# Performance work log

Hardware: AMD Instinct MI355X
Metric: run time of the kernel (lower is better)

Reference implementation:

```python
import jax, jax.numpy as jnp
import numpy as np

HEAD_SIZE = 64


def setup_inputs() -> dict:
    key = jax.random.key(0)
    k1, k2, k3, k4 = jax.random.split(key, 4)
    B, T, C = 4, 4096, 1024
    x = jax.random.normal(k1, (B, T, C), dtype=jnp.float32)
    s = 1.0 / np.sqrt(C)  # ~kaiming-uniform scale for Linear weights
    Wk = jax.random.normal(k2, (C, HEAD_SIZE), dtype=jnp.float32) * s
    Wq = jax.random.normal(k3, (C, HEAD_SIZE), dtype=jnp.float32) * s
    Wv = jax.random.normal(k4, (C, HEAD_SIZE), dtype=jnp.float32) * s
    return {"x": x, "Wk": Wk, "Wq": Wq, "Wv": Wv}


def reference(x, Wk, Wq, Wv):
    # x: [B,T,C]; Wk/Wq/Wv: [C,H]
    B, T, C = x.shape
    H = Wk.shape[1]
    k = jnp.einsum('btc,ch->bth', x, Wk)
    q = jnp.einsum('btc,ch->bth', x, Wq)
    v = jnp.einsum('btc,ch->bth', x, Wv)
    scale = 1.0 / jnp.sqrt(jnp.asarray(H, dtype=x.dtype))
    scores = jnp.einsum('bqh,bkh->bqk', q, k) * scale  # [B,T,T]
    causal = jnp.tril(jnp.ones((T, T), dtype=bool))
    scores = jnp.where(causal, scores, jnp.asarray(-jnp.inf, dtype=scores.dtype))
    attn = jax.nn.softmax(scores, axis=-1)
    out = jnp.einsum('bqk,bkh->bqh', attn, v)  # [B,T,H]
    return out
```

## Files before the change

kernel.cpp:

```cpp
#include <hip/hip_runtime.h>
#include <hip/hip_bf16.h>

#define T_ 4096
#define C_ 1024
#define H_ 64
#define LSTR 72
#define XBS 1032

typedef short bf16x8 __attribute__((ext_vector_type(8)));
typedef float f32x4 __attribute__((ext_vector_type(4)));

__device__ __forceinline__ short f2bf(float f) {
  union { __hip_bfloat16 h; short s; } u;
  u.h = __float2bfloat16(f);
  return u.s;
}
__device__ __forceinline__ unsigned pack2(float a, float b) {
  return ((unsigned)(unsigned short)f2bf(b) << 16) | (unsigned short)f2bf(a);
}

__global__ void wtrans_kernel(const float* __restrict__ Wk,
                              const float* __restrict__ Wq,
                              const float* __restrict__ Wv,
                              __hip_bfloat16* __restrict__ Wtf) {
  int tid = blockIdx.x * 256 + threadIdx.x;
  const int j = tid & 7;
  const int lane = (tid >> 3) & 63;
  const int m = lane & 15;
  const int quad = lane >> 4;
  const int f = (tid >> 9) & 15;
  const int nt = f & 3;
  const int ks = f >> 2;
  const int c = (tid >> 13) & 7;
  const int which = tid >> 16;
  const float* W = (which == 0) ? Wk : ((which == 1) ? Wq : Wv);
  const int cc = c * 128 + ks * 32 + quad * 8 + j;
  const int h = nt * 16 + m;
  Wtf[tid] = __float2bfloat16(W[cc * 64 + h]);
}

__global__ __launch_bounds__(256) void proj_kernel(
    const float* __restrict__ x, const __hip_bfloat16* __restrict__ Wtf,
    __hip_bfloat16* __restrict__ qb, __hip_bfloat16* __restrict__ Kf,
    __hip_bfloat16* __restrict__ Vf) {
  __shared__ __hip_bfloat16 Xb[16 * XBS];
  const int tid = threadIdx.x;
  const int lane = tid & 63;
  const int wave = tid >> 6;
  const int m = lane & 15;
  const int quad = lane >> 4;
  const int t0 = blockIdx.x * 16;

  const float4* xtile = (const float4*)(x + (size_t)t0 * C_);
  float4 xv[16];
#pragma unroll
  for (int k = 0; k < 16; ++k) xv[k] = xtile[tid + k * 256];
#pragma unroll
  for (int k = 0; k < 16; ++k) {
    const int idx = tid + k * 256;
    const int row = idx >> 8;
    const int c4 = idx & 255;
    uint2 u = {pack2(xv[k].x, xv[k].y), pack2(xv[k].z, xv[k].w)};
    *(uint2*)(&Xb[row * XBS + c4 * 4]) = u;
  }
  __syncthreads();

  int whichs[3], ntls[3];
  const __hip_bfloat16* wb[3];
#pragma unroll
  for (int i = 0; i < 3; ++i) {
    const int g = wave * 3 + i;
    whichs[i] = g >> 2;
    ntls[i] = g & 3;
    wb[i] = Wtf + (size_t)whichs[i] * 65536 + ntls[i] * 512 + lane * 8;
  }
  f32x4 acc[3];
#pragma unroll
  for (int i = 0; i < 3; ++i) acc[i] = (f32x4){0.f, 0.f, 0.f, 0.f};

#pragma unroll
  for (int c = 0; c < 8; ++c) {
    bf16x8 bq[12];
#pragma unroll
    for (int i = 0; i < 3; ++i)
#pragma unroll
      for (int ks = 0; ks < 4; ++ks)
        bq[i * 4 + ks] = *(const bf16x8*)(wb[i] + (c * 16 + ks * 4) * 512);
#pragma unroll
    for (int ks = 0; ks < 4; ++ks) {
      bf16x8 a = *(const bf16x8*)(&Xb[m * XBS + c * 128 + ks * 32 + quad * 8]);
#pragma unroll
      for (int i = 0; i < 3; ++i)
        acc[i] = __builtin_amdgcn_mfma_f32_16x16x32_bf16(a, bq[i * 4 + ks],
                                                         acc[i], 0, 0, 0);
    }
  }

  const int bb = t0 >> 12;
  const int tloc = t0 & (T_ - 1);
  const int ktile = tloc >> 6;
  const float cscale = 0.18033688011112042f;

#pragma unroll
  for (int i = 0; i < 3; ++i) {
    const int which = whichs[i];
    const int ntl = ntls[i];
    if (which == 1) {
#pragma unroll
      for (int r = 0; r < 4; ++r)
        qb[(size_t)(t0 + quad * 4 + r) * H_ + ntl * 16 + m] =
            __float2bfloat16(acc[i][r] * cscale);
    } else if (which == 0) {
      __hip_bfloat16* dst = Kf + ((size_t)bb * 64 + ktile) * 4096;
      const int ntK = (tloc >> 4) & 3;
      const int wh = ntl >> 1;
      const int quadK = (ntl * 2 + (m >> 3)) & 3;
      const int j = m & 7;
#pragma unroll
      for (int r = 0; r < 4; ++r) {
        const int mK = quad * 4 + r;
        dst[(ntK * 2 + wh) * 512 + (quadK * 16 + mK) * 8 + j] =
            __float2bfloat16(acc[i][r]);
      }
    } else {
      __hip_bfloat16* dst = Vf + ((size_t)bb * 64 + ktile) * 4096;
#pragma unroll
      for (int r = 0; r < 4; ++r) {
        const int kvo = (tloc & 63) + quad * 4 + r;
        const int half = (kvo >> 5) & 1;
        const int quadV = (kvo >> 3) & 3;
        const int j = kvo & 7;
        dst[(ntl * 2 + half) * 512 + (quadV * 16 + m) * 8 + j] =
            __float2bfloat16(acc[i][r]);
      }
    }
  }
}

__global__ __launch_bounds__(256, 4) void fa_pass1(
    const __hip_bfloat16* __restrict__ qg, const __hip_bfloat16* __restrict__ Kf,
    const __hip_bfloat16* __restrict__ Vf, float* __restrict__ Opart,
    float* __restrict__ Ml) {
  __shared__ __hip_bfloat16 Pl[4][16 * LSTR];
  const int lane = threadIdx.x & 63;
  const int wave = threadIdx.x >> 6;
  const int m = lane & 15;
  const int quad = lane >> 4;

  const int jid = blockIdx.x * 4 + wave;
  const int b = jid / 1152;
  const int j2 = jid - b * 1152;
  int g = 7;
  while (16 * g * (g + 1) > j2) --g;
  const int r2 = j2 - 16 * g * (g + 1);
  const int qt = 32 * g + r2 / (g + 1);
  const int c = r2 - (r2 / (g + 1)) * (g + 1);
  const int q0 = qt * 16;
  const int k0s = c * 512;
  const int kend0 = k0s + 512;
  const int kend = (kend0 < q0 + 16) ? kend0 : (q0 + 16);
  const int ntile = (kend - k0s + 63) >> 6;

  const __hip_bfloat16* qbase = qg + ((size_t)b * T_ + q0 + m) * H_;
  bf16x8 qf0 = *(const bf16x8*)(qbase + quad * 8);
  bf16x8 qf1 = *(const bf16x8*)(qbase + 32 + quad * 8);

  f32x4 Oacc[4];
#pragma unroll
  for (int i = 0; i < 4; ++i) Oacc[i] = (f32x4){0.f, 0.f, 0.f, 0.f};
  float psum = 0.f;

  const __hip_bfloat16* kgf = Kf + (size_t)b * 262144 + lane * 8;
  const __hip_bfloat16* vgf = Vf + (size_t)b * 262144 + lane * 8;
  __hip_bfloat16* Plw = &Pl[wave][0];

  for (int it = 0; it < ntile; ++it) {
    const int ktile = (k0s >> 6) + it;
    const int k0 = ktile * 64;
    const __hip_bfloat16* kp = kgf + (size_t)ktile * 4096;
    const __hip_bfloat16* vp = vgf + (size_t)ktile * 4096;

    f32x4 s[4];
#pragma unroll
    for (int nt = 0; nt < 4; ++nt) {
      bf16x8 kf0 = *(const bf16x8*)(kp + nt * 1024);
      bf16x8 kf1 = *(const bf16x8*)(kp + nt * 1024 + 512);
      f32x4 t = (f32x4){0.f, 0.f, 0.f, 0.f};
      t = __builtin_amdgcn_mfma_f32_16x16x32_bf16(kf0, qf0, t, 0, 0, 0);
      t = __builtin_amdgcn_mfma_f32_16x16x32_bf16(kf1, qf1, t, 0, 0, 0);
      s[nt] = t;
    }
    bf16x8 vf[8];
#pragma unroll
    for (int nt = 0; nt < 4; ++nt) {
      vf[2 * nt] = *(const bf16x8*)(vp + nt * 1024);
      vf[2 * nt + 1] = *(const bf16x8*)(vp + nt * 1024 + 512);
    }

    const bool needmask = (k0 + 63 > q0);
#pragma unroll
    for (int nt = 0; nt < 4; ++nt) {
      float p[4];
#pragma unroll
      for (int r = 0; r < 4; ++r) {
        float sv = s[nt][r];
        if (needmask && (k0 + nt * 16 + quad * 4 + r) > (q0 + m))
          sv = -__builtin_inff();
        p[r] = exp2f(sv);
        psum += p[r];
      }
      uint2 u = {pack2(p[0], p[1]), pack2(p[2], p[3])};
      *(uint2*)(&Plw[m * LSTR + nt * 16 + quad * 4]) = u;
    }

    bf16x8 pf0 = *(const bf16x8*)(&Plw[m * LSTR + quad * 8]);
    bf16x8 pf1 = *(const bf16x8*)(&Plw[m * LSTR + 32 + quad * 8]);
#pragma unroll
    for (int nt = 0; nt < 4; ++nt) {
      Oacc[nt] = __builtin_amdgcn_mfma_f32_16x16x32_bf16(pf0, vf[2 * nt], Oacc[nt], 0, 0, 0);
      Oacc[nt] = __builtin_amdgcn_mfma_f32_16x16x32_bf16(pf1, vf[2 * nt + 1], Oacc[nt], 0, 0, 0);
    }
  }

  psum += __shfl_xor(psum, 16);
  psum += __shfl_xor(psum, 32);

  float* Op = Opart + (size_t)jid * 1024;
#pragma unroll
  for (int nt = 0; nt < 4; ++nt)
#pragma unroll
    for (int r = 0; r < 4; ++r)
      Op[(quad * 4 + r) * 64 + nt * 16 + m] = Oacc[nt][r];
  if (lane < 16) Ml[(size_t)jid * 16 + lane] = psum;
}

__global__ __launch_bounds__(256) void fa_combine(
    const float* __restrict__ Opart, const float* __restrict__ Ml,
    float* __restrict__ out) {
  const int bq = blockIdx.x;
  const int b = bq >> 8;
  const int qt = bq & 255;
  const int g = qt >> 5;
  const int nc = g + 1;
  const int jbase = b * 1152 + 16 * g * (g + 1) + (qt & 31) * nc;
  const int r = threadIdx.x >> 4;
  const int h0 = (threadIdx.x & 15) * 4;

  float4 O = {0.f, 0.f, 0.f, 0.f};
  float L = 0.f;
  for (int c = 0; c < nc; ++c) {
    L += Ml[(size_t)(jbase + c) * 16 + r];
    float4 o = *(const float4*)(Opart + (size_t)(jbase + c) * 1024 + r * 64 + h0);
    O.x += o.x; O.y += o.y; O.z += o.z; O.w += o.w;
  }
  float inv = 1.f / L;
  float4 res = {O.x * inv, O.y * inv, O.z * inv, O.w * inv};
  *(float4*)(out + ((size_t)b * T_ + qt * 16 + r) * H_ + h0) = res;
}

extern "C" void kernel_launch(void* const* d_in, const int* in_sizes, int n_in,
                              void* d_out, int out_size, void* d_ws, size_t ws_size,
                              hipStream_t stream) {
  const float* x = (const float*)d_in[0];
  const float* Wk = (const float*)d_in[1];
  const float* Wq = (const float*)d_in[2];
  const float* Wv = (const float*)d_in[3];
  float* out = (float*)d_out;
  char* ws = (char*)d_ws;
  __hip_bfloat16* Wtf = (__hip_bfloat16*)ws;
  __hip_bfloat16* qb = (__hip_bfloat16*)(ws + 393216);
  __hip_bfloat16* Kf = (__hip_bfloat16*)(ws + 2490368);
  __hip_bfloat16* Vf = (__hip_bfloat16*)(ws + 4587520);
  float* Opart = (float*)(ws + 6684672);
  float* Ml = (float*)(ws + 25559040);

  hipLaunchKernelGGL(wtrans_kernel, dim3(768), dim3(256), 0, stream, Wk, Wq, Wv, Wtf);
  hipLaunchKernelGGL(proj_kernel, dim3(1024), dim3(256), 0, stream, x, Wtf, qb, Kf, Vf);
  hipLaunchKernelGGL(fa_pass1, dim3(1152), dim3(256), 0, stream, qb, Kf, Vf, Opart, Ml);
  hipLaunchKernelGGL(fa_combine, dim3(1024), dim3(256), 0, stream, Opart, Ml, out);
}
```

Measured before the change: 144.9 us.

## Prefetch next K tile, double-buffer P, and combine partials with atomics

The attention pass now loads the next K tile into registers while computing the current one, and ping-pongs the per-wave P staging buffer in LDS. Split-K partial outputs and row sums are no longer written to a partials buffer and reduced by a combine kernel. They are atomically accumulated into a zeroed final buffer, and a simple normalize kernel divides by the sum. This adds a memset, lowers the occupancy hint from 4 to 3, and relies on float atomics, which make summation order non-deterministic.

```diff
diff --git a/kernel.cpp b/kernel.cpp
--- a/kernel.cpp
+++ b/kernel.cpp
@@ -137,11 +137,11 @@
   }
 }
 
-__global__ __launch_bounds__(256, 4) void fa_pass1(
+__global__ __launch_bounds__(256, 3) void fa_pass1(
     const __hip_bfloat16* __restrict__ qg, const __hip_bfloat16* __restrict__ Kf,
-    const __hip_bfloat16* __restrict__ Vf, float* __restrict__ Opart,
-    float* __restrict__ Ml) {
-  __shared__ __hip_bfloat16 Pl[4][16 * LSTR];
+    const __hip_bfloat16* __restrict__ Vf, float* __restrict__ Ofin,
+    float* __restrict__ Lfin) {
+  __shared__ __hip_bfloat16 Pl[4][2][16 * LSTR];
   const int lane = threadIdx.x & 63;
   const int wave = threadIdx.x >> 6;
   const int m = lane & 15;
@@ -160,6 +160,7 @@
   const int kend0 = k0s + 512;
   const int kend = (kend0 < q0 + 16) ? kend0 : (q0 + 16);
   const int ntile = (kend - k0s + 63) >> 6;
+  const int kt0 = k0s >> 6;
 
   const __hip_bfloat16* qbase = qg + ((size_t)b * T_ + q0 + m) * H_;
   bf16x8 qf0 = *(const bf16x8*)(qbase + quad * 8);
@@ -172,31 +173,47 @@
 
   const __hip_bfloat16* kgf = Kf + (size_t)b * 262144 + lane * 8;
   const __hip_bfloat16* vgf = Vf + (size_t)b * 262144 + lane * 8;
-  __hip_bfloat16* Plw = &Pl[wave][0];
+
+  bf16x8 kf[8];
+  {
+    const __hip_bfloat16* kp = kgf + (size_t)kt0 * 4096;
+#pragma unroll
+    for (int nt = 0; nt < 4; ++nt) {
+      kf[2 * nt] = *(const bf16x8*)(kp + nt * 1024);
+      kf[2 * nt + 1] = *(const bf16x8*)(kp + nt * 1024 + 512);
+    }
+  }
 
   for (int it = 0; it < ntile; ++it) {
-    const int ktile = (k0s >> 6) + it;
+    const int ktile = kt0 + it;
     const int k0 = ktile * 64;
-    const __hip_bfloat16* kp = kgf + (size_t)ktile * 4096;
     const __hip_bfloat16* vp = vgf + (size_t)ktile * 4096;
 
-    f32x4 s[4];
-#pragma unroll
-    for (int nt = 0; nt < 4; ++nt) {
-      bf16x8 kf0 = *(const bf16x8*)(kp + nt * 1024);
-      bf16x8 kf1 = *(const bf16x8*)(kp + nt * 1024 + 512);
-      f32x4 t = (f32x4){0.f, 0.f, 0.f, 0.f};
-      t = __builtin_amdgcn_mfma_f32_16x16x32_bf16(kf0, qf0, t, 0, 0, 0);
-      t = __builtin_amdgcn_mfma_f32_16x16x32_bf16(kf1, qf1, t, 0, 0, 0);
-      s[nt] = t;
-    }
     bf16x8 vf[8];
 #pragma unroll
     for (int nt = 0; nt < 4; ++nt) {
       vf[2 * nt] = *(const bf16x8*)(vp + nt * 1024);
       vf[2 * nt + 1] = *(const bf16x8*)(vp + nt * 1024 + 512);
     }
-
+    const int ktn = (it + 1 < ntile) ? (ktile + 1) : ktile;
+    const __hip_bfloat16* kpn = kgf + (size_t)ktn * 4096;
+    bf16x8 kn[8];
+#pragma unroll
+    for (int nt = 0; nt < 4; ++nt) {
+      kn[2 * nt] = *(const bf16x8*)(kpn + nt * 1024);
+      kn[2 * nt + 1] = *(const bf16x8*)(kpn + nt * 1024 + 512);
+    }
+
+    f32x4 s[4];
+#pragma unroll
+    for (int nt = 0; nt < 4; ++nt) {
+      f32x4 t = (f32x4){0.f, 0.f, 0.f, 0.f};
+      t = __builtin_amdgcn_mfma_f32_16x16x32_bf16(kf[2 * nt], qf0, t, 0, 0, 0);
+      t = __builtin_amdgcn_mfma_f32_16x16x32_bf16(kf[2 * nt + 1], qf1, t, 0, 0, 0);
+      s[nt] = t;
+    }
+
+    __hip_bfloat16* Plw = &Pl[wave][it & 1][0];
     const bool needmask = (k0 + 63 > q0);
 #pragma unroll
     for (int nt = 0; nt < 4; ++nt) {
@@ -220,42 +237,31 @@
       Oacc[nt] = __builtin_amdgcn_mfma_f32_16x16x32_bf16(pf0, vf[2 * nt], Oacc[nt], 0, 0, 0);
       Oacc[nt] = __builtin_amdgcn_mfma_f32_16x16x32_bf16(pf1, vf[2 * nt + 1], Oacc[nt], 0, 0, 0);
     }
+#pragma unroll
+    for (int i = 0; i < 8; ++i) kf[i] = kn[i];
   }
 
   psum += __shfl_xor(psum, 16);
   psum += __shfl_xor(psum, 32);
 
-  float* Op = Opart + (size_t)jid * 1024;
+  float* Og = Ofin + ((size_t)b * T_ + q0) * 64;
 #pragma unroll
   for (int nt = 0; nt < 4; ++nt)
 #pragma unroll
     for (int r = 0; r < 4; ++r)
-      Op[(quad * 4 + r) * 64 + nt * 16 + m] = Oacc[nt][r];
-  if (lane < 16) Ml[(size_t)jid * 16 + lane] = psum;
-}
-
-__global__ __launch_bounds__(256) void fa_combine(
-    const float* __restrict__ Opart, const float* __restrict__ Ml,
+      atomicAdd(&Og[(quad * 4 + r) * 64 + nt * 16 + m], Oacc[nt][r]);
+  if (lane < 16) atomicAdd(&Lfin[(size_t)b * T_ + q0 + lane], psum);
+}
+
+__global__ __launch_bounds__(256) void fa_norm(
+    const float* __restrict__ Ofin, const float* __restrict__ Lfin,
     float* __restrict__ out) {
-  const int bq = blockIdx.x;
-  const int b = bq >> 8;
-  const int qt = bq & 255;
-  const int g = qt >> 5;
-  const int nc = g + 1;
-  const int jbase = b * 1152 + 16 * g * (g + 1) + (qt & 31) * nc;
-  const int r = threadIdx.x >> 4;
-  const int h0 = (threadIdx.x & 15) * 4;
-
-  float4 O = {0.f, 0.f, 0.f, 0.f};
-  float L = 0.f;
-  for (int c = 0; c < nc; ++c) {
-    L += Ml[(size_t)(jbase + c) * 16 + r];
-    float4 o = *(const float4*)(Opart + (size_t)(jbase + c) * 1024 + r * 64 + h0);
-    O.x += o.x; O.y += o.y; O.z += o.z; O.w += o.w;
-  }
-  float inv = 1.f / L;
-  float4 res = {O.x * inv, O.y * inv, O.z * inv, O.w * inv};
-  *(float4*)(out + ((size_t)b * T_ + qt * 16 + r) * H_ + h0) = res;
+  const int idx = blockIdx.x * 256 + threadIdx.x;
+  const int row = idx >> 4;
+  float inv = 1.f / Lfin[row];
+  float4 o = ((const float4*)Ofin)[idx];
+  float4 res = {o.x * inv, o.y * inv, o.z * inv, o.w * inv};
+  ((float4*)out)[idx] = res;
 }
 
 extern "C" void kernel_launch(void* const* d_in, const int* in_sizes, int n_in,
@@ -271,11 +277,12 @@
   __hip_bfloat16* qb = (__hip_bfloat16*)(ws + 393216);
   __hip_bfloat16* Kf = (__hip_bfloat16*)(ws + 2490368);
   __hip_bfloat16* Vf = (__hip_bfloat16*)(ws + 4587520);
-  float* Opart = (float*)(ws + 6684672);
-  float* Ml = (float*)(ws + 25559040);
-
+  float* Ofin = (float*)(ws + 6684672);
+  float* Lfin = (float*)(ws + 6684672 + 4194304);
+
+  hipMemsetAsync(Ofin, 0, 4194304 + 65536, stream);
   hipLaunchKernelGGL(wtrans_kernel, dim3(768), dim3(256), 0, stream, Wk, Wq, Wv, Wtf);
   hipLaunchKernelGGL(proj_kernel, dim3(1024), dim3(256), 0, stream, x, Wtf, qb, Kf, Vf);
-  hipLaunchKernelGGL(fa_pass1, dim3(1152), dim3(256), 0, stream, qb, Kf, Vf, Opart, Ml);
-  hipLaunchKernelGGL(fa_combine, dim3(1024), dim3(256), 0, stream, Opart, Ml, out);
-}
+  hipLaunchKernelGGL(fa_pass1, dim3(1152), dim3(256), 0, stream, qb, Kf, Vf, Ofin, Lfin);
+  hipLaunchKernelGGL(fa_norm, dim3(1024), dim3(256), 0, stream, Ofin, Lfin, out);
+}
```

Result: no change. 147.7 us (+1.9%).
